# Kernel optimization log

Measured on AMD Instinct MI355X. Metric: run time of the kernel, lower is better.

Reference implementation:

```python
import jax, jax.numpy as jnp
import numpy as np

N0, N1, N2 = 200000, 50000, 10000
E0, E1 = 750000, 150000
D_IN, HID, OUT = 256, 256, 64


def _sage_conv(x_src, x_tgt, src, dst, Wl, bl, Wr, n_tgt):
    # PyG SAGEConv(aggr='mean'): lin_l(mean of neighbor msgs) + lin_r(x_tgt)
    msgs = x_src[src]                                   # [E, D] gather
    s = jax.ops.segment_sum(msgs, dst, num_segments=n_tgt)           # [n_tgt, D]
    cnt = jax.ops.segment_sum(jnp.ones((src.shape[0], 1), x_src.dtype), dst,
                              num_segments=n_tgt)                    # [n_tgt, 1]
    agg = jnp.where(cnt > 0, s / jnp.maximum(cnt, 1.0), 0.0)
    return agg @ Wl + bl + x_tgt @ Wr


def setup_inputs() -> dict:
    key = jax.random.key(0)
    ks = jax.random.split(key, 12)
    inv = lambda d: 1.0 / np.sqrt(d)
    return {
        "x": jax.random.normal(ks[0], (N0, D_IN), jnp.float32),
        "src0": jax.random.randint(ks[1], (E0,), 0, N0),
        "dst0": jax.random.randint(ks[2], (E0,), 0, N1),
        "src1": jax.random.randint(ks[3], (E1,), 0, N1),
        "dst1": jax.random.randint(ks[4], (E1,), 0, N2),
        "Wl0": jax.random.uniform(ks[5], (D_IN, HID), jnp.float32, -inv(D_IN), inv(D_IN)),
        "bl0": jnp.zeros((HID,), jnp.float32),
        "Wr0": jax.random.uniform(ks[6], (D_IN, HID), jnp.float32, -inv(D_IN), inv(D_IN)),
        "Wl1": jax.random.uniform(ks[7], (HID, HID), jnp.float32, -inv(HID), inv(HID)),
        "bl1": jnp.zeros((HID,), jnp.float32),
        "Wr1": jax.random.uniform(ks[8], (HID, HID), jnp.float32, -inv(HID), inv(HID)),
        "Wlin": jax.random.uniform(ks[9], (HID, OUT), jnp.float32, -inv(HID), inv(HID)),
        "blin": jnp.zeros((OUT,), jnp.float32),
        "n_tgt0": N1,
        "n_tgt1": N2,
    }


def reference(x, src0, dst0, src1, dst1, Wl0, bl0, Wr0, Wl1, bl1, Wr1, Wlin, blin,
              n_tgt0, n_tgt1):
    # layer 0: N0 sources -> n_tgt0 targets, then relu (dropout = identity in eval)
    h = _sage_conv(x, x[:n_tgt0], src0, dst0, Wl0, bl0, Wr0, n_tgt0)
    h = jax.nn.relu(h)
    # layer 1 (last): -> n_tgt1 targets, then tanh
    h = _sage_conv(h, h[:n_tgt1], src1, dst1, Wl1, bl1, Wr1, n_tgt1)
    h = jnp.tanh(h)
    logits = h @ Wlin + blin
    return jax.nn.softmax(logits, axis=1)
```

## Files before the change

kernel.cpp:

```cpp
#include <hip/hip_runtime.h>
#include <math.h>

#define N0 200000
#define N1 50000
#define N2 10000
#define E0 750000
#define E1 150000
#define D 256
#define OUT 64
#define CAP 64

#define BM 64
#define BN 128
#define FS_ROWS 32

#define FILL_B 3516
#define PACK_B 512
#define CAST_B 50000

typedef unsigned int uint32;
using short8 = __attribute__((ext_vector_type(8))) short;
using f32x4 = __attribute__((ext_vector_type(4))) float;

__device__ __forceinline__ unsigned short bf16_rne(float f) {
    unsigned int u = __float_as_uint(f);
    unsigned int r = (u + 0x7FFFu + ((u >> 16) & 1u)) >> 16;
    return (unsigned short)r;
}
__device__ __forceinline__ float bf16_f32(unsigned short h) {
    return __uint_as_float(((unsigned int)h) << 16);
}

__device__ __forceinline__ void gload_lds16(const void* g, void* l) {
    __builtin_amdgcn_global_load_lds(
        (const __attribute__((address_space(1))) unsigned int*)g,
        (__attribute__((address_space(3))) unsigned int*)l, 16, 0, 0);
}

__global__ void prep(const float* __restrict__ x, unsigned short* __restrict__ xhi,
                     const int* __restrict__ src0, const int* __restrict__ dst0,
                     int* __restrict__ cnt0, int* __restrict__ eidx0,
                     const int* __restrict__ src1, const int* __restrict__ dst1,
                     int* __restrict__ cnt1, int* __restrict__ eidx1,
                     const float* __restrict__ Wl0, const float* __restrict__ Wr0,
                     unsigned short* __restrict__ WThi0, unsigned short* __restrict__ WTlo0,
                     const float* __restrict__ Wl1, const float* __restrict__ Wr1,
                     unsigned short* __restrict__ WThi1, unsigned short* __restrict__ WTlo1) {
    int b = blockIdx.x;
    if (b < FILL_B) {
        int e = b * 256 + threadIdx.x;
        if (e < E0) {
            int d = dst0[e];
            int pos = atomicAdd(&cnt0[d], 1);
            if (pos < CAP) eidx0[d * CAP + pos] = src0[e];
        } else if (e < E0 + E1) {
            int e1 = e - E0;
            int d = dst1[e1];
            int pos = atomicAdd(&cnt1[d], 1);
            if (pos < CAP) eidx1[d * CAP + pos] = src1[e1];
        }
    } else if (b < FILL_B + PACK_B) {
        int pb = b - FILL_B;
        int layer = pb >> 8;
        int n = pb & 255;
        const float* Wl = layer ? Wl1 : Wl0;
        const float* Wr = layer ? Wr1 : Wr0;
        unsigned short* WThi = layer ? WThi1 : WThi0;
        unsigned short* WTlo = layer ? WTlo1 : WTlo0;
        #pragma unroll
        for (int kc = threadIdx.x; kc < 512; kc += 256) {
            float v = (kc < 256) ? Wl[(size_t)kc * D + n] : Wr[(size_t)(kc - 256) * D + n];
            unsigned short h = bf16_rne(v);
            WThi[(size_t)n * 512 + kc] = h;
            WTlo[(size_t)n * 512 + kc] = bf16_rne(v - bf16_f32(h));
        }
    } else {
        int i = (b - FILL_B - PACK_B) * 256 + threadIdx.x;
        float4 v = *reinterpret_cast<const float4*>(x + (size_t)i * 4);
        ushort4 h;
        h.x = bf16_rne(v.x); h.y = bf16_rne(v.y);
        h.z = bf16_rne(v.z); h.w = bf16_rne(v.w);
        *reinterpret_cast<ushort4*>(xhi + (size_t)i * 4) = h;
    }
}

__global__ void aggregate_h(const unsigned short* __restrict__ srcHi,
                            const int* __restrict__ cnt, const int* __restrict__ eidx,
                            unsigned short* __restrict__ aggHi, int T) {
    int wave = threadIdx.x >> 6;
    int lane = threadIdx.x & 63;
    int t = blockIdx.x * 4 + wave;
    if (t >= T) return;
    int deg = cnt[t];
    int n = deg < CAP ? deg : CAP;
    int vidx = eidx[(size_t)t * CAP + lane];
    float a0 = 0.f, a1 = 0.f, a2 = 0.f, a3 = 0.f;

    for (int j0 = 0; j0 < n; j0 += 4) {
        int   s[4];
        float w[4];
        #pragma unroll
        for (int jj = 0; jj < 4; ++jj) {
            int j = j0 + jj;
            int sv = __shfl(vidx, j);
            bool act = j < n;
            s[jj] = act ? sv : 0;
            w[jj] = act ? 1.f : 0.f;
        }
        ushort4 uh[4];
        #pragma unroll
        for (int jj = 0; jj < 4; ++jj)
            uh[jj] = *reinterpret_cast<const ushort4*>(srcHi + (size_t)s[jj] * D + lane * 4);
        #pragma unroll
        for (int jj = 0; jj < 4; ++jj) {
            a0 += w[jj] * bf16_f32(uh[jj].x);
            a1 += w[jj] * bf16_f32(uh[jj].y);
            a2 += w[jj] * bf16_f32(uh[jj].z);
            a3 += w[jj] * bf16_f32(uh[jj].w);
        }
    }

    float sc = deg > 0 ? 1.0f / (float)deg : 0.0f;
    ushort4 oh;
    oh.x = bf16_rne(a0 * sc); oh.y = bf16_rne(a1 * sc);
    oh.z = bf16_rne(a2 * sc); oh.w = bf16_rne(a3 * sc);
    *reinterpret_cast<ushort4*>(aggHi + (size_t)t * D + lane * 4) = oh;
}

template<int ACT>
__global__ void __launch_bounds__(256, 4)
gemm_split(const unsigned short* __restrict__ A1hi, const unsigned short* __restrict__ A2hi,
           const unsigned short* __restrict__ WThi, const unsigned short* __restrict__ WTlo,
           const float* __restrict__ bias, unsigned short* __restrict__ Chi,
           float* __restrict__ Cf, int M) {
    __shared__ __align__(16) char sAhi[BM * 128];
    __shared__ __align__(16) char sBhi[BN * 128];
    __shared__ __align__(16) char sBlo[BN * 128];

    const int tid = threadIdx.x;
    const int m0 = blockIdx.x * BM;
    const int n0 = blockIdx.y * BN;
    const int wid = tid >> 6, lane = tid & 63;
    const int lr = lane & 15;
    const int hi2 = lane >> 4;

    const int srow = lane >> 3;
    const int scol = ((lane & 7) ^ srow) << 4;

    f32x4 acc[4][2];
    #pragma unroll
    for (int i = 0; i < 4; ++i)
        #pragma unroll
        for (int j = 0; j < 2; ++j)
            acc[i][j] = (f32x4){0.f, 0.f, 0.f, 0.f};

    for (int k0 = 0; k0 < 512; k0 += 64) {
        if (k0) __syncthreads();
        const char* Ah = (const char*)((k0 < 256) ? A1hi : A2hi);
        const int kc = k0 & 255;
        #pragma unroll
        for (int i = 0; i < 2; ++i) {
            int ch = wid * 2 + i;
            int row = ch * 8 + srow;
            size_t ga = ((size_t)(m0 + row) * D + kc) * 2 + scol;
            gload_lds16(Ah + ga, sAhi + ch * 1024);
        }
        #pragma unroll
        for (int i = 0; i < 4; ++i) {
            int ch = wid * 4 + i;
            int row = ch * 8 + srow;
            size_t gb = ((size_t)(n0 + row) * 512 + k0) * 2 + scol;
            gload_lds16((const char*)WThi + gb, sBhi + ch * 1024);
            gload_lds16((const char*)WTlo + gb, sBlo + ch * 1024);
        }
        __syncthreads();

        #pragma unroll
        for (int slab = 0; slab < 2; ++slab) {
            const int z = slab * 64 + hi2 * 16;
            short8 ah[4], bh[2], bl[2];
            #pragma unroll
            for (int f = 0; f < 4; ++f) {
                int ra = f * 16 + lr;
                int oa = ra * 128 + (z ^ ((ra & 7) << 4));
                ah[f] = *reinterpret_cast<const short8*>(sAhi + oa);
            }
            #pragma unroll
            for (int f = 0; f < 2; ++f) {
                int rb = wid * 32 + f * 16 + lr;
                int ob = rb * 128 + (z ^ ((rb & 7) << 4));
                bh[f] = *reinterpret_cast<const short8*>(sBhi + ob);
                bl[f] = *reinterpret_cast<const short8*>(sBlo + ob);
            }
            #pragma unroll
            for (int i = 0; i < 4; ++i)
                #pragma unroll
                for (int j = 0; j < 2; ++j) {
                    acc[i][j] = __builtin_amdgcn_mfma_f32_16x16x32_bf16(ah[i], bh[j], acc[i][j], 0, 0, 0);
                    acc[i][j] = __builtin_amdgcn_mfma_f32_16x16x32_bf16(ah[i], bl[j], acc[i][j], 0, 0, 0);
                }
        }
    }

    #pragma unroll
    for (int fn = 0; fn < 2; ++fn) {
        int col = n0 + wid * 32 + fn * 16 + lr;
        float bv = bias[col];
        #pragma unroll
        for (int fm = 0; fm < 4; ++fm) {
            int rbase = m0 + fm * 16 + hi2 * 4;
            #pragma unroll
            for (int r = 0; r < 4; ++r) {
                int m = rbase + r;
                if (m < M) {
                    float v = acc[fm][fn][r] + bv;
                    if (ACT == 0) {
                        Chi[(size_t)m * D + col] = bf16_rne(fmaxf(v, 0.f));
                    } else {
                        Cf[(size_t)m * D + col] = tanhf(v);
                    }
                }
            }
        }
    }
}

__global__ void __launch_bounds__(256)
final_softmax(const float* __restrict__ H, const float* __restrict__ Wlin,
              const float* __restrict__ blin, float* __restrict__ out, int M) {
    __shared__ __align__(16) float sW[D * OUT];
    const int tid = threadIdx.x;
    #pragma unroll
    for (int i = 0; i < 16; ++i) {
        int idx = (i * 256 + tid) * 4;
        *reinterpret_cast<float4*>(&sW[idx]) = *reinterpret_cast<const float4*>(&Wlin[idx]);
    }
    __syncthreads();

    const int wave = tid >> 6, lane = tid & 63;
    const float bl = blin[lane];
    int r0 = blockIdx.x * FS_ROWS + wave * (FS_ROWS / 4);
    int r1 = r0 + FS_ROWS / 4;
    for (int r = r0; r < r1 && r < M; ++r) {
        const float* hrow = H + (size_t)r * D;
        float a0 = 0.f, a1 = 0.f, a2 = 0.f, a3 = 0.f;
        #pragma unroll 8
        for (int k = 0; k < D; k += 4) {
            a0 += hrow[k + 0] * sW[(k + 0) * OUT + lane];
            a1 += hrow[k + 1] * sW[(k + 1) * OUT + lane];
            a2 += hrow[k + 2] * sW[(k + 2) * OUT + lane];
            a3 += hrow[k + 3] * sW[(k + 3) * OUT + lane];
        }
        float acc = (a0 + a1) + (a2 + a3) + bl;
        float mx = acc;
        #pragma unroll
        for (int off = 32; off > 0; off >>= 1) mx = fmaxf(mx, __shfl_xor(mx, off));
        float e = __expf(acc - mx);
        float s = e;
        #pragma unroll
        for (int off = 32; off > 0; off >>= 1) s += __shfl_xor(s, off);
        out[(size_t)r * OUT + lane] = e / s;
    }
}

extern "C" void kernel_launch(void* const* d_in, const int* in_sizes, int n_in,
                              void* d_out, int out_size, void* d_ws, size_t ws_size,
                              hipStream_t stream) {
    const float* x    = (const float*)d_in[0];
    const int*   src0 = (const int*)d_in[1];
    const int*   dst0 = (const int*)d_in[2];
    const int*   src1 = (const int*)d_in[3];
    const int*   dst1 = (const int*)d_in[4];
    const float* Wl0  = (const float*)d_in[5];
    const float* bl0  = (const float*)d_in[6];
    const float* Wr0  = (const float*)d_in[7];
    const float* Wl1  = (const float*)d_in[8];
    const float* bl1  = (const float*)d_in[9];
    const float* Wr1  = (const float*)d_in[10];
    const float* Wlin = (const float*)d_in[11];
    const float* blin = (const float*)d_in[12];

    const int PADX = 200064;
    const int PAD1 = 50048;
    const int PAD2 = 10112;

    char* ws = (char*)d_ws;
    size_t off = 0;
    auto alloc = [&](size_t bytes) {
        void* p = ws + off;
        off += (bytes + 255) & ~(size_t)255;
        return p;
    };
    int* cnt0  = (int*)alloc((size_t)N1 * 4);
    int* cnt1  = (int*)alloc((size_t)N2 * 4);
    size_t cnt_span = (size_t)((char*)cnt1 - (char*)cnt0) + (size_t)N2 * 4;
    int* eidx0 = (int*)alloc((size_t)N1 * CAP * 4);
    int* eidx1 = (int*)alloc((size_t)N2 * CAP * 4);
    unsigned short* agg0hi = (unsigned short*)alloc((size_t)PAD1 * D * 2);
    unsigned short* xhi    = (unsigned short*)alloc((size_t)PADX * D * 2);
    unsigned short* h0hi   = (unsigned short*)alloc((size_t)N1 * D * 2);
    unsigned short* agg1hi = (unsigned short*)alloc((size_t)PAD2 * D * 2);
    float* h1f = (float*)alloc((size_t)N2 * D * 4);
    unsigned short* WThi0 = (unsigned short*)alloc((size_t)D * 512 * 2);
    unsigned short* WTlo0 = (unsigned short*)alloc((size_t)D * 512 * 2);
    unsigned short* WThi1 = (unsigned short*)alloc((size_t)D * 512 * 2);
    unsigned short* WTlo1 = (unsigned short*)alloc((size_t)D * 512 * 2);

    hipMemsetAsync(cnt0, 0, cnt_span, stream);

    prep<<<FILL_B + PACK_B + CAST_B, 256, 0, stream>>>(
        x, xhi, src0, dst0, cnt0, eidx0, src1, dst1, cnt1, eidx1,
        Wl0, Wr0, WThi0, WTlo0, Wl1, Wr1, WThi1, WTlo1);

    aggregate_h<<<(N1 + 3) / 4, 256, 0, stream>>>(xhi, cnt0, eidx0, agg0hi, N1);
    gemm_split<0><<<dim3((N1 + BM - 1) / BM, 2), 256, 0, stream>>>(
        agg0hi, xhi, WThi0, WTlo0, bl0, h0hi, (float*)nullptr, N1);

    aggregate_h<<<(N2 + 3) / 4, 256, 0, stream>>>(h0hi, cnt1, eidx1, agg1hi, N2);
    gemm_split<1><<<dim3((N2 + BM - 1) / BM, 2), 256, 0, stream>>>(
        agg1hi, h0hi, WThi1, WTlo1, bl1, (unsigned short*)nullptr, h1f, N2);

    final_softmax<<<(N2 + FS_ROWS - 1) / FS_ROWS, 256, 0, stream>>>(
        h1f, Wlin, blin, (float*)d_out, N2);
}
```

Baseline: 272.2 us.

## Interleave vectorized edge-fill blocks among cast blocks in prep kernel

The CSR-fill work in the prep kernel now has each thread handle four edges through int4 loads, which cuts the number of fill blocks by four. The fill blocks are also spread evenly across the grid, one in every 58 blocks, instead of sitting at the front. The goal is to overlap the latency-bound atomic scatter with the bandwidth-bound bf16 cast of x, so the atomics do not run as one serialized phase. The block-index remapping adds some integer division and makes the code harder to follow.

```diff
diff --git a/kernel.cpp b/kernel.cpp
--- a/kernel.cpp
+++ b/kernel.cpp
@@ -14,9 +14,11 @@
 #define BN 128
 #define FS_ROWS 32
 
-#define FILL_B 3516
+#define CAST_B 50000
 #define PACK_B 512
-#define CAST_B 50000
+#define FILL4_B 879
+#define ISTRIDE 58
+#define GRID_B (CAST_B + PACK_B + FILL4_B)
 
 typedef unsigned int uint32;
 using short8 = __attribute__((ext_vector_type(8))) short;
@@ -47,40 +49,61 @@
                      const float* __restrict__ Wl1, const float* __restrict__ Wr1,
                      unsigned short* __restrict__ WThi1, unsigned short* __restrict__ WTlo1) {
     int b = blockIdx.x;
-    if (b < FILL_B) {
-        int e = b * 256 + threadIdx.x;
-        if (e < E0) {
-            int d = dst0[e];
-            int pos = atomicAdd(&cnt0[d], 1);
-            if (pos < CAP) eidx0[d * CAP + pos] = src0[e];
-        } else if (e < E0 + E1) {
-            int e1 = e - E0;
-            int d = dst1[e1];
-            int pos = atomicAdd(&cnt1[d], 1);
-            if (pos < CAP) eidx1[d * CAP + pos] = src1[e1];
-        }
-    } else if (b < FILL_B + PACK_B) {
-        int pb = b - FILL_B;
-        int layer = pb >> 8;
-        int n = pb & 255;
-        const float* Wl = layer ? Wl1 : Wl0;
-        const float* Wr = layer ? Wr1 : Wr0;
-        unsigned short* WThi = layer ? WThi1 : WThi0;
-        unsigned short* WTlo = layer ? WTlo1 : WTlo0;
-        #pragma unroll
-        for (int kc = threadIdx.x; kc < 512; kc += 256) {
-            float v = (kc < 256) ? Wl[(size_t)kc * D + n] : Wr[(size_t)(kc - 256) * D + n];
-            unsigned short h = bf16_rne(v);
-            WThi[(size_t)n * 512 + kc] = h;
-            WTlo[(size_t)n * 512 + kc] = bf16_rne(v - bf16_f32(h));
+    int k = b / ISTRIDE;
+    bool isfill = ((b % ISTRIDE) == ISTRIDE - 1) && (k < FILL4_B);
+    if (isfill) {
+        int e0 = k * 1024 + threadIdx.x * 4;
+        if (e0 < E0) {
+            int4 dv = *reinterpret_cast<const int4*>(dst0 + e0);
+            int4 sv = *reinterpret_cast<const int4*>(src0 + e0);
+            int p0 = atomicAdd(&cnt0[dv.x], 1);
+            int p1 = atomicAdd(&cnt0[dv.y], 1);
+            int p2 = atomicAdd(&cnt0[dv.z], 1);
+            int p3 = atomicAdd(&cnt0[dv.w], 1);
+            if (p0 < CAP) eidx0[dv.x * CAP + p0] = sv.x;
+            if (p1 < CAP) eidx0[dv.y * CAP + p1] = sv.y;
+            if (p2 < CAP) eidx0[dv.z * CAP + p2] = sv.z;
+            if (p3 < CAP) eidx0[dv.w * CAP + p3] = sv.w;
+        } else if (e0 < E0 + E1) {
+            int e1 = e0 - E0;
+            int4 dv = *reinterpret_cast<const int4*>(dst1 + e1);
+            int4 sv = *reinterpret_cast<const int4*>(src1 + e1);
+            int p0 = atomicAdd(&cnt1[dv.x], 1);
+            int p1 = atomicAdd(&cnt1[dv.y], 1);
+            int p2 = atomicAdd(&cnt1[dv.z], 1);
+            int p3 = atomicAdd(&cnt1[dv.w], 1);
+            if (p0 < CAP) eidx1[dv.x * CAP + p0] = sv.x;
+            if (p1 < CAP) eidx1[dv.y * CAP + p1] = sv.y;
+            if (p2 < CAP) eidx1[dv.z * CAP + p2] = sv.z;
+            if (p3 < CAP) eidx1[dv.w * CAP + p3] = sv.w;
         }
     } else {
-        int i = (b - FILL_B - PACK_B) * 256 + threadIdx.x;
-        float4 v = *reinterpret_cast<const float4*>(x + (size_t)i * 4);
-        ushort4 h;
-        h.x = bf16_rne(v.x); h.y = bf16_rne(v.y);
-        h.z = bf16_rne(v.z); h.w = bf16_rne(v.w);
-        *reinterpret_cast<ushort4*>(xhi + (size_t)i * 4) = h;
+        int nf = (b + 1) / ISTRIDE;
+        if (nf > FILL4_B) nf = FILL4_B;
+        int r = b - nf;
+        if (r < CAST_B) {
+            int i = r * 256 + threadIdx.x;
+            float4 v = *reinterpret_cast<const float4*>(x + (size_t)i * 4);
+            ushort4 h;
+            h.x = bf16_rne(v.x); h.y = bf16_rne(v.y);
+            h.z = bf16_rne(v.z); h.w = bf16_rne(v.w);
+            *reinterpret_cast<ushort4*>(xhi + (size_t)i * 4) = h;
+        } else {
+            int pb = r - CAST_B;
+            int layer = pb >> 8;
+            int n = pb & 255;
+            const float* Wl = layer ? Wl1 : Wl0;
+            const float* Wr = layer ? Wr1 : Wr0;
+            unsigned short* WThi = layer ? WThi1 : WThi0;
+            unsigned short* WTlo = layer ? WTlo1 : WTlo0;
+            #pragma unroll
+            for (int kc = threadIdx.x; kc < 512; kc += 256) {
+                float v = (kc < 256) ? Wl[(size_t)kc * D + n] : Wr[(size_t)(kc - 256) * D + n];
+                unsigned short h = bf16_rne(v);
+                WThi[(size_t)n * 512 + kc] = h;
+                WTlo[(size_t)n * 512 + kc] = bf16_rne(v - bf16_f32(h));
+            }
+        }
     }
 }
 
@@ -308,7 +331,7 @@
 
     hipMemsetAsync(cnt0, 0, cnt_span, stream);
 
-    prep<<<FILL_B + PACK_B + CAST_B, 256, 0, stream>>>(
+    prep<<<GRID_B, 256, 0, stream>>>(
         x, xhi, src0, dst0, cnt0, eidx0, src1, dst1, cnt1, eidx1,
         Wl0, Wr0, WThi0, WTlo0, Wl1, Wr1, WThi1, WTlo1);
 
```

Result: faster. 263.8 us (-3.1%).
